# Kernel optimization log

Hardware: AMD Instinct MI355X
Metric: run time of the kernel (lower is better)

Reference implementation:

```python
import jax, jax.numpy as jnp
import numpy as np

N_WAY = 5
K_SHOT = 1
QUERY = 75          # queries per class -> 375 total
PRJ = 14            # projections per support class
C, H, W = 512, 10, 10
NUM_NODE = H * W
SINK_EPS = 0.05     # entropic regularization (on max-normalized cost)
SINK_ITERS = 50


def setup_inputs() -> dict:
    key = jax.random.key(0)
    k1, k2 = jax.random.split(key)
    n_support = N_WAY * K_SHOT * PRJ
    num_query = N_WAY * QUERY
    feat = jax.random.normal(k1, (n_support + num_query, C, H, W), dtype=jnp.float32)
    label = jax.random.randint(k2, (num_query,), 0, N_WAY)
    return {"feat": feat, "label": label}


def _sinkhorn(cost, r, c, eps=SINK_EPS, iters=SINK_ITERS):
    """Batched entropic OT (log-domain Sinkhorn), replacing the per-pair
    cv2.EMD CPU solve. cost: [..., n, m]; r: [..., n]; c: [..., m].
    r and c each sum to NUM_NODE, so total transported mass is NUM_NODE,
    matching the cv2.EMD flow scale. Scaling the cost by a positive scalar
    does not change the (exact-)OT plan, so we max-normalize per pair for a
    consistent effective regularization."""
    scale = jnp.max(cost, axis=(-1, -2), keepdims=True) + 1e-6
    cost = cost / scale
    log_r = jnp.log(r)
    log_c = jnp.log(c)

    def body(fg, _):
        f, g = fg
        f = eps * (log_r - jax.nn.logsumexp((g[..., None, :] - cost) / eps, axis=-1))
        g = eps * (log_c - jax.nn.logsumexp((f[..., :, None] - cost) / eps, axis=-2))
        return (f, g), None

    init = (jnp.zeros_like(r), jnp.zeros_like(c))
    (f, g), _ = jax.lax.scan(body, init, None, length=iters)
    return jnp.exp((f[..., :, None] + g[..., None, :] - cost) / eps)


def reference(feat, label):
    n_support = N_WAY * K_SHOT * PRJ
    support = feat[:n_support].reshape(N_WAY, PRJ, C, H, W)
    query = feat[n_support:]                       # [nq, C, H, W]
    proto = support.mean(axis=1)                   # [way, C, H, W]
    nq = query.shape[0]

    # --- get_weight_vector: <A_node_feat, global_avg(B)> per (A,B) pair ---
    proto_avg = proto.mean(axis=(2, 3))            # [way, C]
    query_avg = query.mean(axis=(2, 3))            # [nq, C]
    qf = query.reshape(nq, C, NUM_NODE)
    pf = proto.reshape(N_WAY, C, NUM_NODE)
    w1 = jax.nn.relu(jnp.einsum('mcp,nc->mnp', qf, proto_avg)) + 0.001  # [nq, way, N]
    w2 = jax.nn.relu(jnp.einsum('ncp,mc->nmp', pf, query_avg)) + 0.001  # [way, nq, N]

    # --- normalize_feature: subtract channel mean ---
    protoN = proto - proto.mean(axis=1, keepdims=True)
    queryN = query - query.mean(axis=1, keepdims=True)

    # --- similarity map: 1 - squared L2 over channels, per node pair ---
    p = protoN.reshape(N_WAY, C, NUM_NODE).transpose(0, 2, 1)  # [way, N, C]
    q = queryN.reshape(nq, C, NUM_NODE).transpose(0, 2, 1)     # [nq, N, C]
    qn = (q ** 2).sum(-1)                                      # [nq, N]
    pn = (p ** 2).sum(-1)                                      # [way, N]
    cross = jnp.einsum('iac,jbc->ijab', q, p)                  # [nq, way, N, N]
    sqd = qn[:, None, :, None] + pn[None, :, None, :] - 2.0 * cross
    sim = 1.0 - sqd                                            # similarity_map
    cost = sqd                                                 # = 1 - sim

    # --- marginal weights, normalized to sum NUM_NODE (as in emd_inference) ---
    ww1 = jax.nn.relu(w1) + 1e-5
    ww1 = ww1 * (NUM_NODE / ww1.sum(-1, keepdims=True))        # [nq, way, N]
    ww2 = jax.nn.relu(jnp.transpose(w2, (1, 0, 2))) + 1e-5     # weight_2[j,i] -> [nq, way, N]
    ww2 = ww2 * (NUM_NODE / ww2.sum(-1, keepdims=True))

    # --- OT flow (detached, like torch.from_numpy(flow)) ---
    flow = jax.lax.stop_gradient(
        _sinkhorn(jax.lax.stop_gradient(cost), jax.lax.stop_gradient(ww1), jax.lax.stop_gradient(ww2))
    )

    temperature = 12.5 / NUM_NODE
    logits = (sim * flow).sum((-1, -2)) * temperature          # [nq, way]
    log_p_y = jax.nn.log_softmax(logits, axis=1)
    loss = -jnp.take_along_axis(log_p_y, label[:, None], axis=1).mean()
    return (log_p_y, loss)
```

## Files before the change

### kernel.cpp

```cpp
#include <hip/hip_runtime.h>
#include <math.h>

#define NW   5
#define PRJ  14
#define CCH  512
#define PP   100
#define NQ   375
#define NS   70
#define NPAIR (NQ*NW)

#define OFF_PROTO   0
#define OFF_PAVG    256000
#define OFF_QAVG    258560
#define OFF_QSQ     450560
#define OFF_PSQ     488060
#define OFF_LOGITS  488560
#define OFF_PF16    490440

typedef float f32x16 __attribute__((ext_vector_type(16)));
typedef _Float16 f16x2 __attribute__((ext_vector_type(2)));
typedef _Float16 f16x8 __attribute__((ext_vector_type(8)));

__device__ __forceinline__ int SWZ(int n) { return n ^ ((n >> 2) & 7); }

__global__ void k_proto(const float* __restrict__ feat, float* __restrict__ ws) {
    int nc = blockIdx.x;
    int n  = nc >> 9;
    int p  = threadIdx.x;
    float s = 0.f;
    if (p < PP) {
        const float* base = feat + (size_t)((n * PRJ) * CCH) * PP + (size_t)(nc & 511) * PP + p;
        #pragma unroll
        for (int k = 0; k < PRJ; ++k) s += base[(size_t)k * CCH * PP];
        s *= (1.f / PRJ);
        ws[OFF_PROTO + nc * PP + p] = s;
    }
    float v = (p < PP) ? s : 0.f;
    #pragma unroll
    for (int off = 32; off; off >>= 1) v += __shfl_down(v, off);
    __shared__ float red[2];
    if ((threadIdx.x & 63) == 0) red[threadIdx.x >> 6] = v;
    __syncthreads();
    if (threadIdx.x == 0) ws[OFF_PAVG + nc] = (red[0] + red[1]) * (1.f / PP);
}

__global__ __launch_bounds__(256) void k_qstat(const float* __restrict__ src,
                                               float* __restrict__ dst_sq,
                                               float* __restrict__ dst_avg) {
    __shared__ __align__(16) float t[6400];
    int b = blockIdx.x, tid = threadIdx.x;
    const float* base = src + (size_t)b * CCH * PP;
    float qsq = 0.f;
    for (int c0 = 0; c0 < CCH; c0 += 64) {
        __syncthreads();
        const float4* g = (const float4*)(base + (size_t)c0 * PP);
        for (int i = tid; i < 1600; i += 256) ((float4*)t)[i] = g[i];
        __syncthreads();
        if (tid < PP) {
            #pragma unroll 8
            for (int c = 0; c < 64; ++c) { float x = t[c * PP + tid]; qsq = fmaf(x, x, qsq); }
        } else if (tid >= 128 && tid < 192) {
            int ch = tid - 128;
            const float4* row = (const float4*)(t + ch * PP);
            float s = 0.f;
            #pragma unroll
            for (int i = 0; i < 25; ++i) { float4 v = row[i]; s += (v.x + v.y) + (v.z + v.w); }
            if (dst_avg) dst_avg[(size_t)b * CCH + c0 + ch] = s * (1.f / PP);
        }
    }
    if (tid < PP) dst_sq[b * PP + tid] = qsq;
}

__global__ __launch_bounds__(256) void k_pconv(float* __restrict__ ws) {
    int b = blockIdx.x;
    int n = b >> 4, kt = b & 15;
    int tid = threadIdx.x;
    int c0 = kt * 32;
    uint* img = (uint*)(ws + OFF_PF16) + (size_t)b * 2048;
    const float* pb = ws + OFF_PROTO + (size_t)n * CCH * PP;
    const float* pavg = ws + OFF_PAVG + n * CCH;
    for (int i = tid; i < 1600; i += 256) {
        int cp = i / 100, col = i - cp * 100;
        float a0 = pb[(size_t)(c0 + 2 * cp) * PP + col];
        float a1 = pb[(size_t)(c0 + 2 * cp + 1) * PP + col];
        uint pk = __builtin_bit_cast(uint, __builtin_amdgcn_cvt_pkrtz(a0, a1));
        img[(((cp >> 2) << 7) | SWZ(col)) * 4 + (cp & 3)] = pk;
    }
    if (tid < 16) {
        int cp = tid;
        float a0 = pavg[c0 + 2 * cp], a1 = pavg[c0 + 2 * cp + 1];
        uint pk = __builtin_bit_cast(uint, __builtin_amdgcn_cvt_pkrtz(a0, a1));
        img[(((cp >> 2) << 7) | 101) * 4 + (cp & 3)] = pk;
    }
    for (int i = tid; i < 448; i += 256) {
        int dw = i & 3; int t2 = i >> 2;
        int s_i = t2 % 28; int k4 = t2 / 28;
        int s = 100 + s_i;
        if (s == 101) continue;
        img[(((k4) << 7) | s) * 4 + dw] = (s == 100) ? 0x3C003C00u : 0u;
    }
}

__global__ __launch_bounds__(256, 4) void k_pair(const float* __restrict__ query,
                                                 float* __restrict__ ws) {
    __shared__ __align__(16) char SH[22400];
    __shared__ __align__(16) uint uh[56], vh[56];
    __shared__ float wrL[PP], wcL[PP], qnl[PP], pnl[PP], sqv[PP], spv[PP];
    __shared__ float red[8];

    uint* Kst = (uint*)SH;

    int p_ = blockIdx.x;
    int xcd = p_ & 7, off_ = p_ >> 3;
    int pair = (xcd < 3) ? (xcd * 235 + off_) : (705 + (xcd - 3) * 234 + off_);

    int m = pair / NW;
    int n = pair - m * NW;
    int tid = threadIdx.x;
    int lane = tid & 63, wid = tid >> 6;
    int lrow = lane & 31, lhi = lane >> 5;

    const float* qb = query + (size_t)m * CCH * PP;
    const float* qavg_g = ws + OFF_QAVG + (size_t)m * CCH;
    const uint* pimg = (const uint*)(ws + OFF_PF16) + (size_t)n * 16 * 2048;

    for (int idx = tid; idx < 112; idx += 256) {
        int s_i = idx % 28; int k4 = idx / 28;
        int s = 100 + s_i;
        if (s == 101) continue;
        uint4 val = (s == 100)
                  ? make_uint4(0x3C003C00u, 0x3C003C00u, 0x3C003C00u, 0x3C003C00u)
                  : make_uint4(0u, 0u, 0u, 0u);
        *(uint4*)&SH[(k4 * 128 + s) * 16] = val;
    }

    f32x16 acc[4];
    #pragma unroll
    for (int tc = 0; tc < 4; ++tc)
        #pragma unroll
        for (int e = 0; e < 16; ++e) acc[tc][e] = 0.f;

    int arow16 = SWZ(32 * wid + lrow) * 16;
    int bcol16[4];
    #pragma unroll
    for (int tc = 0; tc < 4; ++tc) bcol16[tc] = SWZ(32 * tc + lrow) * 16;

    for (int kt = 0; kt < 16; ++kt) {
        int c0 = kt * 32;
        for (int idx = tid; idx < 400; idx += 256) {
            int cp = idx / 25, n4 = idx - cp * 25;
            const float* src = qb + (size_t)(c0 + 2 * cp) * PP + n4 * 4;
            float4 x0 = *(const float4*)src;
            float4 x1 = *(const float4*)(src + PP);
            const float* p0 = (const float*)&x0;
            const float* p1 = (const float*)&x1;
            int basedw = ((cp >> 2) << 7);
            int dwb = (cp & 3) * 4;
            #pragma unroll
            for (int i4 = 0; i4 < 4; ++i4) {
                int node = n4 * 4 + i4;
                uint pk = __builtin_bit_cast(uint, __builtin_amdgcn_cvt_pkrtz(p0[i4], p1[i4]));
                *(uint*)&SH[(basedw + SWZ(node)) * 16 + dwb] = pk;
            }
        }
        if (tid < 16) {
            int cp = tid;
            uint pk = __builtin_bit_cast(uint,
                __builtin_amdgcn_cvt_pkrtz(qavg_g[c0 + 2 * cp], qavg_g[c0 + 2 * cp + 1]));
            *(uint*)&SH[(((cp >> 2) << 7) + 101) * 16 + (cp & 3) * 4] = pk;
        }
        {
            const float4* gB = (const float4*)(pimg + (size_t)kt * 2048);
            float4* sB = (float4*)&SH[8192];
            for (int i = tid; i < 512; i += 256) sB[i] = gB[i];
        }
        __syncthreads();
        __builtin_amdgcn_s_setprio(1);
        #pragma unroll
        for (int s = 0; s < 2; ++s) {
            int kb = (2 * s + lhi) * 2048;
            f16x8 ah = *(const f16x8*)&SH[kb + arow16];
            #pragma unroll
            for (int tc = 0; tc < 4; ++tc) {
                f16x8 bh = *(const f16x8*)&SH[8192 + kb + bcol16[tc]];
                acc[tc] = __builtin_amdgcn_mfma_f32_32x32x16_f16(ah, bh, acc[tc], 0, 0, 0);
            }
        }
        __builtin_amdgcn_s_setprio(0);
        __syncthreads();
    }

    if ((lane & 31) == 4 || (lane & 31) == 5) {
        float* dst = ((lane & 31) == 4) ? wrL : sqv;
        #pragma unroll
        for (int reg = 0; reg < 16; ++reg) {
            int row = 32 * wid + (reg & 3) + 8 * (reg >> 2) + 4 * lhi;
            if (row < PP) dst[row] = acc[3][reg];
        }
    }
    if (wid == 3 && lhi == 1) {
        #pragma unroll
        for (int tc = 0; tc < 4; ++tc) {
            int col = 32 * tc + lrow;
            if (col < PP) { wcL[col] = acc[tc][0]; spv[col] = acc[tc][1]; }
        }
    }
    if (tid < 56) {
        vh[tid] = (tid < 25 || (tid >= 28 && tid < 53)) ? 0x3C003C00u : 0u;
        uh[tid] = 0u;
    }
    __syncthreads();

    float v1 = 0.f, v2 = 0.f;
    if (tid < PP) {
        v1 = fmaxf(wrL[tid], 0.f) + 0.00101f;
        v2 = fmaxf(wcL[tid], 0.f) + 0.00101f;
    }
    float s1 = v1, s2 = v2;
    #pragma unroll
    for (int off = 32; off; off >>= 1) { s1 += __shfl_down(s1, off); s2 += __shfl_down(s2, off); }
    if ((tid & 63) == 0) { red[tid >> 6] = s1; red[4 + (tid >> 6)] = s2; }
    __syncthreads();
    float t1 = red[0] + red[1], t2 = red[4] + red[5];
    if (tid < PP) {
        wrL[tid] = v1 * (100.f / t1) * 4.f;
        wcL[tid] = v2 * (100.f / t2) * 4.f;
        float sq = sqv[tid], sp = spv[tid];
        qnl[tid] = ws[OFF_QSQ + m * PP + tid] - sq * sq * (1.f / 512.f);
        pnl[tid] = ws[OFF_PSQ + n * PP + tid] - sp * sp * (1.f / 512.f);
    }
    __syncthreads();

    float spc[4], pnc[4];
    #pragma unroll
    for (int tc = 0; tc < 4; ++tc) {
        int col = 32 * tc + lrow;
        bool cv = col < PP;
        spc[tc] = cv ? spv[col] : 0.f;
        pnc[tc] = cv ? pnl[col] : 0.f;
    }
    float mymax = -1e30f;
    #pragma unroll
    for (int reg = 0; reg < 16; ++reg) {
        int row = 32 * wid + (reg & 3) + 8 * (reg >> 2) + 4 * lhi;
        bool rv = row < PP;
        float sqr = rv ? sqv[row] : 0.f;
        float qnr = rv ? qnl[row] : 0.f;
        #pragma unroll
        for (int tc = 0; tc < 4; ++tc) {
            float sqd = qnr + pnc[tc] - 2.f * (acc[tc][reg] - sqr * spc[tc] * (1.f / 512.f));
            acc[tc][reg] = sqd;
            int col = 32 * tc + lrow;
            if (rv && col < PP) mymax = fmaxf(mymax, sqd);
        }
    }
    #pragma unroll
    for (int off = 32; off; off >>= 1) mymax = fmaxf(mymax, __shfl_down(mymax, off));
    __syncthreads();
    if (lane == 0) red[wid] = mymax;
    __syncthreads();
    float scale = fmaxf(fmaxf(red[0], red[1]), fmaxf(red[2], red[3])) + 1e-6f;
    float k2 = (1.f / scale) * (20.f * 1.44269504088896f);

    #pragma unroll
    for (int tc = 0; tc < 4; ++tc) {
        float kv[16];
        #pragma unroll
        for (int reg = 0; reg < 16; ++reg) kv[reg] = exp2f(fmaf(-acc[tc][reg], k2, 15.f));
        int col = 32 * tc + lrow;
        #pragma unroll
        for (int reg = 0; reg < 16; ++reg) {
            float pv = __shfl_xor(kv[reg], 1);
            int row = 32 * wid + (reg & 3) + 8 * (reg >> 2) + 4 * lhi;
            if (!(lane & 1) && row < PP && col < PP) {
                int j = col >> 1;
                int dw = (j < 25) ? j : (j + 3);
                uint pk = __builtin_bit_cast(uint, __builtin_amdgcn_cvt_pkrtz(kv[reg], pv));
                Kst[row * 56 + dw] = pk;
            }
        }
    }
    __syncthreads();

    int r_ = tid >> 1, hf = tid & 1;
    bool sact = tid < 200;
    uint Kr[25], KTr[25];
    float wr_own = 0.f, wc_own = 0.f;
    if (sact) {
        const uint* rp = Kst + r_ * 56 + 28 * hf;
        #pragma unroll
        for (int q = 0; q < 25; ++q) Kr[q] = rp[q];
        int j = r_ >> 1;
        int dwc = (j < 25) ? j : (j + 3);
        int sh = (r_ & 1) * 16;
        const uint* cp0 = Kst + (50 * hf) * 56 + dwc;
        #pragma unroll
        for (int q = 0; q < 25; ++q) {
            uint d0 = cp0[(2 * q) * 56];
            uint d1 = cp0[(2 * q + 1) * 56];
            KTr[q] = ((d0 >> sh) & 0xFFFFu) | (((d1 >> sh) & 0xFFFFu) << 16);
        }
        wr_own = wrL[r_];
        wc_own = wcL[r_];
    }
    __syncthreads();

    int tpk = tid >> 2;
    float u_ = 0.f, v_ = 0.f;
    for (int it = 0; it < 50; ++it) {
        if (sact) {
            uint4 vv[7];
            const uint4* vp4 = (const uint4*)(vh + hf * 28);
            #pragma unroll
            for (int i = 0; i < 7; ++i) vv[i] = vp4[i];
            const uint* vw = (const uint*)vv;
            float s = 0.f;
            #pragma unroll
            for (int q = 0; q < 25; ++q)
                s = __builtin_amdgcn_fdot2(__builtin_bit_cast(f16x2, Kr[q]),
                                           __builtin_bit_cast(f16x2, vw[q]), s, false);
            s += __shfl_xor(s, 1);
            u_ = fminf(wr_own * __builtin_amdgcn_rcpf(s), 60000.f);
        }
        {
            float u_nb = __shfl_down(u_, 2);
            if (sact && (tid & 3) == 0)
                uh[tpk + (tpk >= 25 ? 3 : 0)] =
                    __builtin_bit_cast(uint, __builtin_amdgcn_cvt_pkrtz(u_, u_nb));
        }
        __syncthreads();
        if (sact) {
            uint4 uu[7];
            const uint4* up4 = (const uint4*)(uh + hf * 28);
            #pragma unroll
            for (int i = 0; i < 7; ++i) uu[i] = up4[i];
            const uint* uw = (const uint*)uu;
            float s = 0.f;
            #pragma unroll
            for (int q = 0; q < 25; ++q)
                s = __builtin_amdgcn_fdot2(__builtin_bit_cast(f16x2, KTr[q]),
                                           __builtin_bit_cast(f16x2, uw[q]), s, false);
            s += __shfl_xor(s, 1);
            v_ = fminf(wc_own * __builtin_amdgcn_rcpf(s), 60000.f);
        }
        {
            float v_nb = __shfl_down(v_, 2);
            if (sact && (tid & 3) == 0)
                vh[tpk + (tpk >= 25 ? 3 : 0)] =
                    __builtin_bit_cast(uint, __builtin_amdgcn_cvt_pkrtz(v_, v_nb));
        }
        __syncthreads();
    }

    float lsum = 0.f;
    if (sact) {
        const uint* vp = vh + hf * 28;
        float rk2 = scale * (1.f / (20.f * 1.44269504088896f));
        #pragma unroll
        for (int q = 0; q < 25; ++q) {
            f16x2 h = __builtin_bit_cast(f16x2, Kr[q]);
            f16x2 vv = __builtin_bit_cast(f16x2, vp[q]);
            float k0 = (float)h[0], k1 = (float)h[1];
            float sq0 = (15.f - __log2f(k0)) * rk2;
            float sq1 = (15.f - __log2f(k1)) * rk2;
            lsum = fmaf((1.f - sq0) * k0, (float)vv[0], lsum);
            lsum = fmaf((1.f - sq1) * k1, (float)vv[1], lsum);
        }
        lsum *= u_;
    }
    #pragma unroll
    for (int off = 32; off; off >>= 1) lsum += __shfl_down(lsum, off);
    if (lane == 0) red[wid] = lsum;
    __syncthreads();
    if (tid == 0)
        ws[OFF_LOGITS + pair] = ((red[0] + red[1]) + (red[2] + red[3])) * (0.125f / 4.f);
}

__global__ void k_final(const int* __restrict__ label, const float* __restrict__ ws,
                        float* __restrict__ out) {
    int t = threadIdx.x;
    float contrib = 0.f;
    if (t < NQ) {
        float lg[NW];
        #pragma unroll
        for (int n = 0; n < NW; ++n) lg[n] = ws[OFF_LOGITS + t * NW + n];
        float mx = lg[0];
        #pragma unroll
        for (int n = 1; n < NW; ++n) mx = fmaxf(mx, lg[n]);
        float s = 0.f;
        #pragma unroll
        for (int n = 0; n < NW; ++n) s += expf(lg[n] - mx);
        float lse = mx + logf(s);
        int lab = label[t];
        #pragma unroll
        for (int n = 0; n < NW; ++n) {
            float lp = lg[n] - lse;
            out[t * NW + n] = lp;
            if (n == lab) contrib = -lp;
        }
    }
    #pragma unroll
    for (int off = 32; off; off >>= 1) contrib += __shfl_down(contrib, off);
    __shared__ float red[6];
    if ((t & 63) == 0) red[t >> 6] = contrib;
    __syncthreads();
    if (t == 0) {
        float s = 0.f;
        #pragma unroll
        for (int i = 0; i < 6; ++i) s += red[i];
        out[NQ * NW] = s * (1.f / NQ);
    }
}

extern "C" void kernel_launch(void* const* d_in, const int* in_sizes, int n_in,
                              void* d_out, int out_size, void* d_ws, size_t ws_size,
                              hipStream_t stream) {
    const float* feat  = (const float*)d_in[0];
    const int*   label = (const int*)d_in[1];
    float* out = (float*)d_out;
    float* ws  = (float*)d_ws;
    const float* query = feat + (size_t)NS * CCH * PP;

    k_proto<<<NW * CCH, 128, 0, stream>>>(feat, ws);
    k_qstat<<<NQ, 256, 0, stream>>>(query, ws + OFF_QSQ, ws + OFF_QAVG);
    k_qstat<<<NW, 256, 0, stream>>>(ws + OFF_PROTO, ws + OFF_PSQ, (float*)nullptr);
    k_pconv<<<NW * 16, 256, 0, stream>>>(ws);
    k_pair<<<NPAIR, 256, 0, stream>>>(query, ws);
    k_final<<<1, 384, 0, stream>>>(label, ws, out);
}
```

Measured before the change: 233.7 us.

## Split pair kernel into cost kernel and single-wave Sinkhorn kernel

The fused per-pair kernel is split in two. A cost kernel computes the exp-cost matrix K and its transpose in fp16 and writes them plus the marginals and scale to a large global workspace. A separate 64-thread Sinkhorn kernel then loads all of K into registers per lane and runs the 50 iterations within a single wave. This aims to cut the barrier cost of 256-thread blocks during the iterations, but adds a global round trip of about 75 MB and an extra launch. The old fused path is kept as a fallback when the workspace is too small.

```diff
diff --git a/kernel.cpp b/kernel.cpp
--- a/kernel.cpp
+++ b/kernel.cpp
@@ -16,6 +16,9 @@
 #define OFF_PSQ     488060
 #define OFF_LOGITS  488560
 #define OFF_PF16    490440
+#define OFF_AUX     654280
+#define OFF_KG      1036780
+#define REQ_WS_BYTES ((size_t)(OFF_KG + 18750000 + 64) * 4)
 
 typedef float f32x16 __attribute__((ext_vector_type(16)));
 typedef _Float16 f16x2 __attribute__((ext_vector_type(2)));
@@ -101,13 +104,12 @@
     }
 }
 
-__global__ __launch_bounds__(256, 4) void k_pair(const float* __restrict__ query,
+
+__global__ __launch_bounds__(256, 4) void k_cost(const float* __restrict__ query,
                                                  float* __restrict__ ws) {
     __shared__ __align__(16) char SH[22400];
-    __shared__ __align__(16) uint uh[56], vh[56];
     __shared__ float wrL[PP], wcL[PP], qnl[PP], pnl[PP], sqv[PP], spv[PP];
     __shared__ float red[8];
-
     uint* Kst = (uint*)SH;
 
     int p_ = blockIdx.x;
@@ -205,10 +207,6 @@
             if (col < PP) { wcL[col] = acc[tc][0]; spv[col] = acc[tc][1]; }
         }
     }
-    if (tid < 56) {
-        vh[tid] = (tid < 25 || (tid >= 28 && tid < 53)) ? 0x3C003C00u : 0u;
-        uh[tid] = 0u;
-    }
     __syncthreads();
 
     float v1 = 0.f, v2 = 0.f;
@@ -284,6 +282,327 @@
 
     int r_ = tid >> 1, hf = tid & 1;
     bool sact = tid < 200;
+    if (sact) {
+        uint Kr[25], KTr[25];
+        const uint* rp = Kst + r_ * 56 + 28 * hf;
+        #pragma unroll
+        for (int q = 0; q < 25; ++q) Kr[q] = rp[q];
+        int j = r_ >> 1;
+        int dwc = (j < 25) ? j : (j + 3);
+        int sh = (r_ & 1) * 16;
+        const uint* cp0 = Kst + (50 * hf) * 56 + dwc;
+        #pragma unroll
+        for (int q = 0; q < 25; ++q) {
+            uint d0 = cp0[(2 * q) * 56];
+            uint d1 = cp0[(2 * q + 1) * 56];
+            KTr[q] = ((d0 >> sh) & 0xFFFFu) | (((d1 >> sh) & 0xFFFFu) << 16);
+        }
+        uint* kg = (uint*)(ws + OFF_KG) + (size_t)pair * 10000 + (r_ >> 1);
+        int ibR = (r_ & 1) * 50 + 25 * hf;
+        int ibT = 100 + (r_ & 1) * 50 + 25 * hf;
+        #pragma unroll
+        for (int q = 0; q < 25; ++q) kg[(ibR + q) * 50] = Kr[q];
+        #pragma unroll
+        for (int q = 0; q < 25; ++q) kg[(ibT + q) * 50] = KTr[q];
+    }
+    float* aux = ws + OFF_AUX + (size_t)pair * 204;
+    if (tid < PP) { aux[tid] = wrL[tid]; aux[100 + tid] = wcL[tid]; }
+    if (tid == 0) aux[200] = scale;
+}
+
+__global__ __launch_bounds__(64, 2) void k_sink(float* __restrict__ ws) {
+    __shared__ __align__(16) uint uhL[52], vhL[52];
+    int pair = blockIdx.x;
+    int l = threadIdx.x;
+    bool act = l < 50;
+
+    const float* aux = ws + OFF_AUX + (size_t)pair * 204;
+    float wr0 = 0.f, wr1 = 0.f, wc0 = 0.f, wc1 = 0.f;
+    if (act) {
+        wr0 = aux[2 * l]; wr1 = aux[2 * l + 1];
+        wc0 = aux[100 + 2 * l]; wc1 = aux[101 + 2 * l];
+    }
+    float scale = aux[200];
+    float rk2 = scale * (1.f / (20.f * 1.44269504088896f));
+
+    uint K0[50], K1[50], T0[50], T1[50];
+    {
+        const uint* kg = (const uint*)(ws + OFF_KG) + (size_t)pair * 10000 + (l < 50 ? l : 0);
+        #pragma unroll
+        for (int i = 0; i < 50; ++i) K0[i] = kg[i * 50];
+        #pragma unroll
+        for (int i = 0; i < 50; ++i) K1[i] = kg[(50 + i) * 50];
+        #pragma unroll
+        for (int i = 0; i < 50; ++i) T0[i] = kg[(100 + i) * 50];
+        #pragma unroll
+        for (int i = 0; i < 50; ++i) T1[i] = kg[(150 + i) * 50];
+    }
+    if (l < 52) { vhL[l] = (l < 50) ? 0x3C003C00u : 0u; uhL[l] = 0u; }
+    __syncthreads();
+
+    float u0 = 0.f, u1 = 0.f;
+    for (int it = 0; it < 50; ++it) {
+        if (act) {
+            const uint4* vp4 = (const uint4*)vhL;
+            float a0 = 0.f, b0 = 0.f, a1 = 0.f, b1 = 0.f;
+            #pragma unroll
+            for (int d4 = 0; d4 < 12; ++d4) {
+                uint4 V = vp4[d4];
+                a0 = __builtin_amdgcn_fdot2(__builtin_bit_cast(f16x2, K0[4*d4+0]), __builtin_bit_cast(f16x2, V.x), a0, false);
+                b0 = __builtin_amdgcn_fdot2(__builtin_bit_cast(f16x2, K0[4*d4+1]), __builtin_bit_cast(f16x2, V.y), b0, false);
+                a0 = __builtin_amdgcn_fdot2(__builtin_bit_cast(f16x2, K0[4*d4+2]), __builtin_bit_cast(f16x2, V.z), a0, false);
+                b0 = __builtin_amdgcn_fdot2(__builtin_bit_cast(f16x2, K0[4*d4+3]), __builtin_bit_cast(f16x2, V.w), b0, false);
+                a1 = __builtin_amdgcn_fdot2(__builtin_bit_cast(f16x2, K1[4*d4+0]), __builtin_bit_cast(f16x2, V.x), a1, false);
+                b1 = __builtin_amdgcn_fdot2(__builtin_bit_cast(f16x2, K1[4*d4+1]), __builtin_bit_cast(f16x2, V.y), b1, false);
+                a1 = __builtin_amdgcn_fdot2(__builtin_bit_cast(f16x2, K1[4*d4+2]), __builtin_bit_cast(f16x2, V.z), a1, false);
+                b1 = __builtin_amdgcn_fdot2(__builtin_bit_cast(f16x2, K1[4*d4+3]), __builtin_bit_cast(f16x2, V.w), b1, false);
+            }
+            {
+                uint v48 = vhL[48], v49 = vhL[49];
+                a0 = __builtin_amdgcn_fdot2(__builtin_bit_cast(f16x2, K0[48]), __builtin_bit_cast(f16x2, v48), a0, false);
+                b0 = __builtin_amdgcn_fdot2(__builtin_bit_cast(f16x2, K0[49]), __builtin_bit_cast(f16x2, v49), b0, false);
+                a1 = __builtin_amdgcn_fdot2(__builtin_bit_cast(f16x2, K1[48]), __builtin_bit_cast(f16x2, v48), a1, false);
+                b1 = __builtin_amdgcn_fdot2(__builtin_bit_cast(f16x2, K1[49]), __builtin_bit_cast(f16x2, v49), b1, false);
+            }
+            u0 = fminf(wr0 * __builtin_amdgcn_rcpf(a0 + b0), 60000.f);
+            u1 = fminf(wr1 * __builtin_amdgcn_rcpf(a1 + b1), 60000.f);
+            uhL[l] = __builtin_bit_cast(uint, __builtin_amdgcn_cvt_pkrtz(u0, u1));
+        }
+        __syncthreads();
+        if (act) {
+            const uint4* up4 = (const uint4*)uhL;
+            float a0 = 0.f, b0 = 0.f, a1 = 0.f, b1 = 0.f;
+            #pragma unroll
+            for (int d4 = 0; d4 < 12; ++d4) {
+                uint4 U = up4[d4];
+                a0 = __builtin_amdgcn_fdot2(__builtin_bit_cast(f16x2, T0[4*d4+0]), __builtin_bit_cast(f16x2, U.x), a0, false);
+                b0 = __builtin_amdgcn_fdot2(__builtin_bit_cast(f16x2, T0[4*d4+1]), __builtin_bit_cast(f16x2, U.y), b0, false);
+                a0 = __builtin_amdgcn_fdot2(__builtin_bit_cast(f16x2, T0[4*d4+2]), __builtin_bit_cast(f16x2, U.z), a0, false);
+                b0 = __builtin_amdgcn_fdot2(__builtin_bit_cast(f16x2, T0[4*d4+3]), __builtin_bit_cast(f16x2, U.w), b0, false);
+                a1 = __builtin_amdgcn_fdot2(__builtin_bit_cast(f16x2, T1[4*d4+0]), __builtin_bit_cast(f16x2, U.x), a1, false);
+                b1 = __builtin_amdgcn_fdot2(__builtin_bit_cast(f16x2, T1[4*d4+1]), __builtin_bit_cast(f16x2, U.y), b1, false);
+                a1 = __builtin_amdgcn_fdot2(__builtin_bit_cast(f16x2, T1[4*d4+2]), __builtin_bit_cast(f16x2, U.z), a1, false);
+                b1 = __builtin_amdgcn_fdot2(__builtin_bit_cast(f16x2, T1[4*d4+3]), __builtin_bit_cast(f16x2, U.w), b1, false);
+            }
+            {
+                uint u48 = uhL[48], u49 = uhL[49];
+                a0 = __builtin_amdgcn_fdot2(__builtin_bit_cast(f16x2, T0[48]), __builtin_bit_cast(f16x2, u48), a0, false);
+                b0 = __builtin_amdgcn_fdot2(__builtin_bit_cast(f16x2, T0[49]), __builtin_bit_cast(f16x2, u49), b0, false);
+                a1 = __builtin_amdgcn_fdot2(__builtin_bit_cast(f16x2, T1[48]), __builtin_bit_cast(f16x2, u48), a1, false);
+                b1 = __builtin_amdgcn_fdot2(__builtin_bit_cast(f16x2, T1[49]), __builtin_bit_cast(f16x2, u49), b1, false);
+            }
+            float v0 = fminf(wc0 * __builtin_amdgcn_rcpf(a0 + b0), 60000.f);
+            float v1n = fminf(wc1 * __builtin_amdgcn_rcpf(a1 + b1), 60000.f);
+            vhL[l] = __builtin_bit_cast(uint, __builtin_amdgcn_cvt_pkrtz(v0, v1n));
+        }
+        __syncthreads();
+    }
+
+    float lsum = 0.f;
+    if (act) {
+        float l0 = 0.f, l1 = 0.f;
+        #pragma unroll
+        for (int d = 0; d < 50; ++d) {
+            f16x2 vv = __builtin_bit_cast(f16x2, vhL[d]);
+            f16x2 h0 = __builtin_bit_cast(f16x2, K0[d]);
+            f16x2 h1 = __builtin_bit_cast(f16x2, K1[d]);
+            float k00 = (float)h0[0], k01 = (float)h0[1];
+            float k10 = (float)h1[0], k11 = (float)h1[1];
+            float v0 = (float)vv[0], v1v = (float)vv[1];
+            l0 = fmaf((1.f - (15.f - __log2f(k00)) * rk2) * k00, v0, l0);
+            l0 = fmaf((1.f - (15.f - __log2f(k01)) * rk2) * k01, v1v, l0);
+            l1 = fmaf((1.f - (15.f - __log2f(k10)) * rk2) * k10, v0, l1);
+            l1 = fmaf((1.f - (15.f - __log2f(k11)) * rk2) * k11, v1v, l1);
+        }
+        lsum = l0 * u0 + l1 * u1;
+    }
+    #pragma unroll
+    for (int off = 32; off; off >>= 1) lsum += __shfl_down(lsum, off);
+    if (l == 0) ws[OFF_LOGITS + pair] = lsum * (0.125f / 4.f);
+}
+
+__global__ __launch_bounds__(256, 4) void k_pair(const float* __restrict__ query,
+                                                 float* __restrict__ ws) {
+    __shared__ __align__(16) char SH[22400];
+    __shared__ __align__(16) uint uh[56], vh[56];
+    __shared__ float wrL[PP], wcL[PP], qnl[PP], pnl[PP], sqv[PP], spv[PP];
+    __shared__ float red[8];
+    uint* Kst = (uint*)SH;
+
+    int p_ = blockIdx.x;
+    int xcd = p_ & 7, off_ = p_ >> 3;
+    int pair = (xcd < 3) ? (xcd * 235 + off_) : (705 + (xcd - 3) * 234 + off_);
+
+    int m = pair / NW;
+    int n = pair - m * NW;
+    int tid = threadIdx.x;
+    int lane = tid & 63, wid = tid >> 6;
+    int lrow = lane & 31, lhi = lane >> 5;
+
+    const float* qb = query + (size_t)m * CCH * PP;
+    const float* qavg_g = ws + OFF_QAVG + (size_t)m * CCH;
+    const uint* pimg = (const uint*)(ws + OFF_PF16) + (size_t)n * 16 * 2048;
+
+    for (int idx = tid; idx < 112; idx += 256) {
+        int s_i = idx % 28; int k4 = idx / 28;
+        int s = 100 + s_i;
+        if (s == 101) continue;
+        uint4 val = (s == 100)
+                  ? make_uint4(0x3C003C00u, 0x3C003C00u, 0x3C003C00u, 0x3C003C00u)
+                  : make_uint4(0u, 0u, 0u, 0u);
+        *(uint4*)&SH[(k4 * 128 + s) * 16] = val;
+    }
+
+    f32x16 acc[4];
+    #pragma unroll
+    for (int tc = 0; tc < 4; ++tc)
+        #pragma unroll
+        for (int e = 0; e < 16; ++e) acc[tc][e] = 0.f;
+
+    int arow16 = SWZ(32 * wid + lrow) * 16;
+    int bcol16[4];
+    #pragma unroll
+    for (int tc = 0; tc < 4; ++tc) bcol16[tc] = SWZ(32 * tc + lrow) * 16;
+
+    for (int kt = 0; kt < 16; ++kt) {
+        int c0 = kt * 32;
+        for (int idx = tid; idx < 400; idx += 256) {
+            int cp = idx / 25, n4 = idx - cp * 25;
+            const float* src = qb + (size_t)(c0 + 2 * cp) * PP + n4 * 4;
+            float4 x0 = *(const float4*)src;
+            float4 x1 = *(const float4*)(src + PP);
+            const float* p0 = (const float*)&x0;
+            const float* p1 = (const float*)&x1;
+            int basedw = ((cp >> 2) << 7);
+            int dwb = (cp & 3) * 4;
+            #pragma unroll
+            for (int i4 = 0; i4 < 4; ++i4) {
+                int node = n4 * 4 + i4;
+                uint pk = __builtin_bit_cast(uint, __builtin_amdgcn_cvt_pkrtz(p0[i4], p1[i4]));
+                *(uint*)&SH[(basedw + SWZ(node)) * 16 + dwb] = pk;
+            }
+        }
+        if (tid < 16) {
+            int cp = tid;
+            uint pk = __builtin_bit_cast(uint,
+                __builtin_amdgcn_cvt_pkrtz(qavg_g[c0 + 2 * cp], qavg_g[c0 + 2 * cp + 1]));
+            *(uint*)&SH[(((cp >> 2) << 7) + 101) * 16 + (cp & 3) * 4] = pk;
+        }
+        {
+            const float4* gB = (const float4*)(pimg + (size_t)kt * 2048);
+            float4* sB = (float4*)&SH[8192];
+            for (int i = tid; i < 512; i += 256) sB[i] = gB[i];
+        }
+        __syncthreads();
+        __builtin_amdgcn_s_setprio(1);
+        #pragma unroll
+        for (int s = 0; s < 2; ++s) {
+            int kb = (2 * s + lhi) * 2048;
+            f16x8 ah = *(const f16x8*)&SH[kb + arow16];
+            #pragma unroll
+            for (int tc = 0; tc < 4; ++tc) {
+                f16x8 bh = *(const f16x8*)&SH[8192 + kb + bcol16[tc]];
+                acc[tc] = __builtin_amdgcn_mfma_f32_32x32x16_f16(ah, bh, acc[tc], 0, 0, 0);
+            }
+        }
+        __builtin_amdgcn_s_setprio(0);
+        __syncthreads();
+    }
+
+    if ((lane & 31) == 4 || (lane & 31) == 5) {
+        float* dst = ((lane & 31) == 4) ? wrL : sqv;
+        #pragma unroll
+        for (int reg = 0; reg < 16; ++reg) {
+            int row = 32 * wid + (reg & 3) + 8 * (reg >> 2) + 4 * lhi;
+            if (row < PP) dst[row] = acc[3][reg];
+        }
+    }
+    if (wid == 3 && lhi == 1) {
+        #pragma unroll
+        for (int tc = 0; tc < 4; ++tc) {
+            int col = 32 * tc + lrow;
+            if (col < PP) { wcL[col] = acc[tc][0]; spv[col] = acc[tc][1]; }
+        }
+    }
+    if (tid < 56) {
+        vh[tid] = (tid < 25 || (tid >= 28 && tid < 53)) ? 0x3C003C00u : 0u;
+        uh[tid] = 0u;
+    }
+    __syncthreads();
+
+    float v1 = 0.f, v2 = 0.f;
+    if (tid < PP) {
+        v1 = fmaxf(wrL[tid], 0.f) + 0.00101f;
+        v2 = fmaxf(wcL[tid], 0.f) + 0.00101f;
+    }
+    float s1 = v1, s2 = v2;
+    #pragma unroll
+    for (int off = 32; off; off >>= 1) { s1 += __shfl_down(s1, off); s2 += __shfl_down(s2, off); }
+    if ((tid & 63) == 0) { red[tid >> 6] = s1; red[4 + (tid >> 6)] = s2; }
+    __syncthreads();
+    float t1 = red[0] + red[1], t2 = red[4] + red[5];
+    if (tid < PP) {
+        wrL[tid] = v1 * (100.f / t1) * 4.f;
+        wcL[tid] = v2 * (100.f / t2) * 4.f;
+        float sq = sqv[tid], sp = spv[tid];
+        qnl[tid] = ws[OFF_QSQ + m * PP + tid] - sq * sq * (1.f / 512.f);
+        pnl[tid] = ws[OFF_PSQ + n * PP + tid] - sp * sp * (1.f / 512.f);
+    }
+    __syncthreads();
+
+    float spc[4], pnc[4];
+    #pragma unroll
+    for (int tc = 0; tc < 4; ++tc) {
+        int col = 32 * tc + lrow;
+        bool cv = col < PP;
+        spc[tc] = cv ? spv[col] : 0.f;
+        pnc[tc] = cv ? pnl[col] : 0.f;
+    }
+    float mymax = -1e30f;
+    #pragma unroll
+    for (int reg = 0; reg < 16; ++reg) {
+        int row = 32 * wid + (reg & 3) + 8 * (reg >> 2) + 4 * lhi;
+        bool rv = row < PP;
+        float sqr = rv ? sqv[row] : 0.f;
+        float qnr = rv ? qnl[row] : 0.f;
+        #pragma unroll
+        for (int tc = 0; tc < 4; ++tc) {
+            float sqd = qnr + pnc[tc] - 2.f * (acc[tc][reg] - sqr * spc[tc] * (1.f / 512.f));
+            acc[tc][reg] = sqd;
+            int col = 32 * tc + lrow;
+            if (rv && col < PP) mymax = fmaxf(mymax, sqd);
+        }
+    }
+    #pragma unroll
+    for (int off = 32; off; off >>= 1) mymax = fmaxf(mymax, __shfl_down(mymax, off));
+    __syncthreads();
+    if (lane == 0) red[wid] = mymax;
+    __syncthreads();
+    float scale = fmaxf(fmaxf(red[0], red[1]), fmaxf(red[2], red[3])) + 1e-6f;
+    float k2 = (1.f / scale) * (20.f * 1.44269504088896f);
+
+    #pragma unroll
+    for (int tc = 0; tc < 4; ++tc) {
+        float kv[16];
+        #pragma unroll
+        for (int reg = 0; reg < 16; ++reg) kv[reg] = exp2f(fmaf(-acc[tc][reg], k2, 15.f));
+        int col = 32 * tc + lrow;
+        #pragma unroll
+        for (int reg = 0; reg < 16; ++reg) {
+            float pv = __shfl_xor(kv[reg], 1);
+            int row = 32 * wid + (reg & 3) + 8 * (reg >> 2) + 4 * lhi;
+            if (!(lane & 1) && row < PP && col < PP) {
+                int j = col >> 1;
+                int dw = (j < 25) ? j : (j + 3);
+                uint pk = __builtin_bit_cast(uint, __builtin_amdgcn_cvt_pkrtz(kv[reg], pv));
+                Kst[row * 56 + dw] = pk;
+            }
+        }
+    }
+    __syncthreads();
+
+    int r_ = tid >> 1, hf = tid & 1;
+    bool sact = tid < 200;
     uint Kr[25], KTr[25];
     float wr_own = 0.f, wc_own = 0.f;
     if (sact) {
@@ -425,6 +744,11 @@
     k_qstat<<<NQ, 256, 0, stream>>>(query, ws + OFF_QSQ, ws + OFF_QAVG);
     k_qstat<<<NW, 256, 0, stream>>>(ws + OFF_PROTO, ws + OFF_PSQ, (float*)nullptr);
     k_pconv<<<NW * 16, 256, 0, stream>>>(ws);
-    k_pair<<<NPAIR, 256, 0, stream>>>(query, ws);
+    if (ws_size >= REQ_WS_BYTES) {
+        k_cost<<<NPAIR, 256, 0, stream>>>(query, ws);
+        k_sink<<<NPAIR, 64, 0, stream>>>(ws);
+    } else {
+        k_pair<<<NPAIR, 256, 0, stream>>>(query, ws);
+    }
     k_final<<<1, 384, 0, stream>>>(label, ws, out);
 }
```

Result: faster. 226.8 us (-2.9%).
